# Performance work log

Hardware: AMD Instinct MI355X
Metric: run time of the kernel (lower is better)

The kernel has to match this reference:

```python
import jax, jax.numpy as jnp
import numpy as np

VOCAB, EMB, HID, L = 100000, 128, 256, 9
B, S = 128, 512
H = HID // 2  # per-direction hidden size
PAD = 0


def setup_inputs() -> dict:
    key = jax.random.key(0)
    ks = jax.random.split(key, 18)
    seqs = jax.random.randint(ks[0], (B, S), 1, VOCAB)
    # left-aligned padding: lengths in [S//2, S]
    lens = jax.random.randint(ks[1], (B,), S // 2, S + 1)
    seqs = jnp.where(jnp.arange(S)[None, :] < lens[:, None], seqs, PAD)
    labels = jax.random.randint(ks[2], (B, S), 0, L)

    def n(k, shape, s=0.05):
        return jax.random.normal(k, shape, jnp.float32) * s

    emb = n(ks[3], (VOCAB, EMB)).at[PAD].set(0.0)
    inp = {
        'sequences': seqs, 'labels': labels, 'emb': emb,
        'w_ih_f': n(ks[4], (4 * H, EMB)), 'w_hh_f': n(ks[5], (4 * H, H)),
        'b_ih_f': n(ks[6], (4 * H,)), 'b_hh_f': n(ks[7], (4 * H,)),
        'w_ih_b': n(ks[8], (4 * H, EMB)), 'w_hh_b': n(ks[9], (4 * H, H)),
        'b_ih_b': n(ks[10], (4 * H,)), 'b_hh_b': n(ks[11], (4 * H,)),
        'w_out': n(ks[12], (L, HID)), 'b_out': n(ks[13], (L,)),
        'start_t': n(ks[14], (L,), 0.1), 'end_t': n(ks[15], (L,), 0.1),
        'trans': n(ks[16], (L, L), 0.1),
    }
    return inp


def _lstm_scan(x, w_ih, w_hh, b_ih, b_hh):
    # x: [S, B, E] -> hidden states [S, B, H]
    h0 = jnp.zeros((x.shape[1], w_hh.shape[1]), x.dtype)

    def step(carry, xt):
        h, c = carry
        g = xt @ w_ih.T + b_ih + h @ w_hh.T + b_hh
        i, f, gg, o = jnp.split(g, 4, axis=-1)  # PyTorch gate order i,f,g,o
        c = jax.nn.sigmoid(f) * c + jax.nn.sigmoid(i) * jnp.tanh(gg)
        h = jax.nn.sigmoid(o) * jnp.tanh(c)
        return (h, c), h

    _, hs = jax.lax.scan(step, (h0, h0), x)
    return hs


def reference(sequences, labels, emb, w_ih_f, w_hh_f, b_ih_f, b_hh_f,
              w_ih_b, w_hh_b, b_ih_b, b_hh_b, w_out, b_out,
              start_t, end_t, trans):
    # Embedding lookup (dropout is identity at inference)
    x = emb[sequences]                      # [B,S,E]
    xt = jnp.swapaxes(x, 0, 1)              # [S,B,E]
    hf = _lstm_scan(xt, w_ih_f, w_hh_f, b_ih_f, b_hh_f)
    hb = _lstm_scan(xt[::-1], w_ih_b, w_hh_b, b_ih_b, b_hh_b)[::-1]
    hcat = jnp.concatenate([hf, hb], axis=-1)         # [S,B,HID]
    emissions = jnp.swapaxes(hcat, 0, 1) @ w_out.T + b_out  # [B,S,L]

    mask = sequences != PAD                 # [B,S], first step all True
    maskf = mask.astype(emissions.dtype)

    # --- CRF numerator (score of gold path) ---
    em_tag = jnp.take_along_axis(emissions, labels[..., None], axis=2)[..., 0]  # [B,S]
    trans_sc = trans[labels[:, :-1], labels[:, 1:]]                              # [B,S-1]
    num = start_t[labels[:, 0]] + em_tag[:, 0] \
        + jnp.sum((trans_sc + em_tag[:, 1:]) * maskf[:, 1:], axis=1)
    seq_ends = jnp.sum(mask, axis=1) - 1
    last_tags = labels[jnp.arange(labels.shape[0]), seq_ends]
    num = num + end_t[last_tags]

    # --- CRF partition function (forward algorithm) ---
    def fstep(score, inp):
        em_t, m_t = inp  # [B,L], [B]
        nxt = jax.nn.logsumexp(score[:, :, None] + trans[None] + em_t[:, None, :], axis=1)
        return jnp.where(m_t[:, None], nxt, score), None

    score0 = start_t[None, :] + emissions[:, 0]  # [B,L]
    em_rest = jnp.swapaxes(emissions, 0, 1)[1:]  # [S-1,B,L]
    scoreT, _ = jax.lax.scan(fstep, score0, (em_rest, mask.T[1:]))
    denom = jax.nn.logsumexp(scoreT + end_t[None, :], axis=1)  # [B]

    # model returns -log_likelihood (torchcrf default reduction='sum')
    return -jnp.sum(num - denom)
```

## Files before the change

kernel.cpp:

```cpp
#include <hip/hip_runtime.h>
#include <hip/hip_bf16.h>

#define B_   128
#define S_   512
#define H_   128
#define G_   512
#define EMB_ 128
#define NL_  9
#define CPW_ 2

typedef __attribute__((ext_vector_type(8))) short bf16x8;
typedef __attribute__((ext_vector_type(4))) short bf16x4;
typedef __attribute__((ext_vector_type(4))) float f32x4;
typedef unsigned short ushort_t;

__device__ __forceinline__ void wg_bar() {
    asm volatile("s_waitcnt lgkmcnt(0)\n\ts_barrier" ::: "memory");
}

__device__ __forceinline__ float bfbits2f(short s) {
    unsigned int u = ((unsigned int)(unsigned short)s) << 16;
    return __builtin_bit_cast(float, u);
}
__device__ __forceinline__ short f2bf(float f) {
    unsigned int u = __builtin_bit_cast(unsigned int, f);
    u += 0x7FFFu + ((u >> 16) & 1u);
    return (short)(u >> 16);
}
__device__ __forceinline__ unsigned int pack2(float lo, float hi) {
    return (unsigned int)(unsigned short)f2bf(lo) | ((unsigned int)(unsigned short)f2bf(hi) << 16);
}
__device__ __forceinline__ float sigm(float x) {
    return __builtin_amdgcn_rcpf(1.f + exp2f(-1.4426950408889634f * x));
}
__device__ __forceinline__ float tanh_(float x) {
    return 1.f - 2.f * __builtin_amdgcn_rcpf(1.f + exp2f(2.8853900817779268f * x));
}

__global__ __launch_bounds__(512, 1)
void xw_gemm_kernel(const int* __restrict__ seq, const float* __restrict__ emb,
                    const float* __restrict__ w_ih_f, const float* __restrict__ b_ih_f,
                    const float* __restrict__ b_hh_f,
                    const float* __restrict__ w_ih_b, const float* __restrict__ b_ih_b,
                    const float* __restrict__ b_hh_b,
                    ushort_t* __restrict__ xw)
{
    __shared__ bf16x8 ldsX[64 * 17];

    const int tid  = threadIdx.x;
    const int wv   = tid >> 6;
    const int n16  = tid & 15;
    const int quad = (tid & 63) >> 4;
    const int dir  = blockIdx.x >> 10;
    const int rem  = blockIdx.x & 1023;
    const int pair = rem >> 4;
    const int tb   = (rem & 15) * 32;

    const float* wih = dir ? w_ih_b : w_ih_f;
    const float* bih = dir ? b_ih_b : b_ih_f;
    const float* bhh = dir ? b_hh_b : b_hh_f;

    {
        int row = tid >> 3, part = tid & 7;
        int b = 2 * pair + (row >> 5);
        int t = tb + (row & 31);
        int tok = seq[b * S_ + t];
        const float* ep = emb + (size_t)tok * EMB_ + part * 16;
        int rt = row >> 4, rr = row & 15;
#pragma unroll
        for (int h = 0; h < 2; h++) {
            float4 a = *(const float4*)(ep + h * 8);
            float4 b4 = *(const float4*)(ep + h * 8 + 4);
            bf16x8 fr;
            fr[0] = f2bf(a.x); fr[1] = f2bf(a.y); fr[2] = f2bf(a.z); fr[3] = f2bf(a.w);
            fr[4] = f2bf(b4.x); fr[5] = f2bf(b4.y); fr[6] = f2bf(b4.z); fr[7] = f2bf(b4.w);
            ldsX[(rt * 16 + part * 2 + h) * 17 + rr] = fr;
        }
    }

    bf16x8 bfrag[4][4];
    float  bias[4];
#pragma unroll
    for (int nt = 0; nt < 4; nt++) {
        int col = nt * 128 + wv * 16 + n16;
        bias[nt] = bih[col] + bhh[col];
#pragma unroll
        for (int ks = 0; ks < 4; ks++) {
            const float* p = wih + col * EMB_ + ks * 32 + quad * 8;
            bf16x8 fr;
#pragma unroll
            for (int j = 0; j < 8; j++) fr[j] = f2bf(p[j]);
            bfrag[nt][ks] = fr;
        }
    }
    __syncthreads();

#pragma unroll
    for (int half = 0; half < 2; half++) {
        f32x4 accA[4], accB[4];
        bf16x8 afA[4], afB[4];
#pragma unroll
        for (int ks = 0; ks < 4; ks++) {
            afA[ks] = ldsX[(half * 16 + ks * 4 + quad) * 17 + n16];
            afB[ks] = ldsX[((half + 2) * 16 + ks * 4 + quad) * 17 + n16];
        }
#pragma unroll
        for (int nt = 0; nt < 4; nt++) {
            f32x4 a = {bias[nt], bias[nt], bias[nt], bias[nt]};
            accA[nt] = a; accB[nt] = a;
#pragma unroll
            for (int ks = 0; ks < 4; ks++) {
                accA[nt] = __builtin_amdgcn_mfma_f32_16x16x32_bf16(afA[ks], bfrag[nt][ks], accA[nt], 0, 0, 0);
                accB[nt] = __builtin_amdgcn_mfma_f32_16x16x32_bf16(afB[ks], bfrag[nt][ks], accB[nt], 0, 0, 0);
            }
        }
#pragma unroll
        for (int r = 0; r < 4; r++) {
            int t = tb + half * 16 + quad * 4 + r;
            int4 iv;
            iv.x = (int)pack2(accA[0][r], accA[1][r]);
            iv.y = (int)pack2(accA[2][r], accA[3][r]);
            iv.z = (int)pack2(accB[0][r], accB[1][r]);
            iv.w = (int)pack2(accB[2][r], accB[3][r]);
            size_t idx = ((((size_t)dir * 64 + pair) * S_ + t) * 8 + wv) * 16 + n16;
            *(int4*)(xw + idx * 8) = iv;
        }
    }
}

#define STEP(K)                                                                    \
  {                                                                                \
    const int u = m16 + (K);                                                       \
    if ((K) == 0 && m < 31) {                                                      \
      const ushort_t* gp = xwp + (size_t)(dir ? (S_ - 32 - m16) : (m16 + 16)) * 1024; \
      sA = *(const int4*)(gp + tid * 8);                                           \
      sB = *(const int4*)(gp + 4096 + tid * 8);                                    \
      sC = *(const int4*)(gp + 8192 + tid * 8);                                    \
      sD = *(const int4*)(gp + 12288 + tid * 8);                                   \
    }                                                                              \
                          \
    bf16x8 af0 = ldsH[(K) & 1][(0  + quad) * 2 + hpar];                            \
    bf16x8 af1 = ldsH[(K) & 1][(4  + quad) * 2 + hpar];                            \
    bf16x8 af2 = ldsH[(K) & 1][(8  + quad) * 2 + hpar];                            \
    bf16x8 af3 = ldsH[(K) & 1][(12 + quad) * 2 + hpar];                            \
    bf16x4 xvg = *(const bf16x4*)(xwS + ((m & 1) * 2048 + ((dir ? (15 - (K)) : (K)) * 8 + wv) * 16 + n16) * 8 + qsel); \
    if ((K) == 8 && m < 31) {                                                      \
      int4* dst = (int4*)(xwL + (((m & 1) ^ 1) * 2048));                           \
      dst[tid] = sA; dst[512 + tid] = sB; dst[1024 + tid] = sC; dst[1536 + tid] = sD; \
    }                                                                              \
    if ((K) == 1 && m >= 1 && (wv == 4 || wv == 5) && lane < 36) {                 \
      int a0 = dir ? (S_ - m16) : (m16 - 16);                                      \
      int eb = (a0 & 31) * 18 + flb;                                               \
      float4 fv;                                                                   \
      fv.x = emL[eb]; fv.y = emL[eb + 2]; fv.z = emL[eb + 4]; fv.w = emL[eb + 6];  \
      *(float4*)(emdir + (size_t)(brow0 + (wv - 4)) * (S_ * NL_) + a0 * NL_ + lane * 4) = fv; \
    }                                                                              \
    f32x4 acc0 = __builtin_amdgcn_mfma_f32_16x16x32_bf16(af0, bfrag[0][0], ZACC, 0, 0, 0); \
    f32x4 acc1 = __builtin_amdgcn_mfma_f32_16x16x32_bf16(af0, bfrag[1][0], ZACC, 0, 0, 0); \
    f32x4 acc2 = __builtin_amdgcn_mfma_f32_16x16x32_bf16(af0, bfrag[2][0], ZACC, 0, 0, 0); \
    f32x4 acc3 = __builtin_amdgcn_mfma_f32_16x16x32_bf16(af0, bfrag[3][0], ZACC, 0, 0, 0); \
    acc0 = __builtin_amdgcn_mfma_f32_16x16x32_bf16(af1, bfrag[0][1], acc0, 0, 0, 0); \
    acc1 = __builtin_amdgcn_mfma_f32_16x16x32_bf16(af1, bfrag[1][1], acc1, 0, 0, 0); \
    acc2 = __builtin_amdgcn_mfma_f32_16x16x32_bf16(af1, bfrag[2][1], acc2, 0, 0, 0); \
    acc3 = __builtin_amdgcn_mfma_f32_16x16x32_bf16(af1, bfrag[3][1], acc3, 0, 0, 0); \
    acc0 = __builtin_amdgcn_mfma_f32_16x16x32_bf16(af2, bfrag[0][2], acc0, 0, 0, 0); \
    acc1 = __builtin_amdgcn_mfma_f32_16x16x32_bf16(af2, bfrag[1][2], acc1, 0, 0, 0); \
    acc2 = __builtin_amdgcn_mfma_f32_16x16x32_bf16(af2, bfrag[2][2], acc2, 0, 0, 0); \
    acc3 = __builtin_amdgcn_mfma_f32_16x16x32_bf16(af2, bfrag[3][2], acc3, 0, 0, 0); \
    acc0 = __builtin_amdgcn_mfma_f32_16x16x32_bf16(af3, bfrag[0][3], acc0, 0, 0, 0); \
    acc1 = __builtin_amdgcn_mfma_f32_16x16x32_bf16(af3, bfrag[1][3], acc1, 0, 0, 0); \
    acc2 = __builtin_amdgcn_mfma_f32_16x16x32_bf16(af3, bfrag[2][3], acc2, 0, 0, 0); \
    acc3 = __builtin_amdgcn_mfma_f32_16x16x32_bf16(af3, bfrag[3][3], acc3, 0, 0, 0); \
    if (wv == 0) {                                                                 \
      f32x4 accE = __builtin_amdgcn_mfma_f32_16x16x32_bf16(af0, bfragE[0], ZACC, 0, 0, 0); \
      accE = __builtin_amdgcn_mfma_f32_16x16x32_bf16(af1, bfragE[1], accE, 0, 0, 0); \
      accE = __builtin_amdgcn_mfma_f32_16x16x32_bf16(af2, bfragE[2], accE, 0, 0, 0); \
      accE = __builtin_amdgcn_mfma_f32_16x16x32_bf16(af3, bfragE[3], accE, 0, 0, 0); \
      if (quad < 2 && n16 < NL_ && u >= 1) {                                       \
        int tprev = dir ? (S_ - u) : (u - 1);                                      \
        emL[((tprev & 31) * 9 + n16) * 2 + quad] = accE[0];                        \
      }                                                                            \
    }                                                                              \
    {                                                                              \
      float gi = acc0[0] + bfbits2f(xvg[0]);                                       \
      float gf = acc1[0] + bfbits2f(xvg[1]);                                       \
      float gg = acc2[0] + bfbits2f(xvg[2]);                                       \
      float go = acc3[0] + bfbits2f(xvg[3]);                                       \
      cst = sigm(gf) * cst + sigm(gi) * tanh_(gg);                                 \
      float hv = sigm(go) * tanh_(cst);                                            \
      if (quad < 2) *(((K) & 1) ? hw0 : hw1) = f2bf(hv);                           \
    }                                                                              \
    wg_bar();                                                                      \
  }

__global__ __launch_bounds__(512, 1)
void lstm_kernel(const ushort_t* __restrict__ xw,
                 const float* __restrict__ w_hh_f, const float* __restrict__ w_hh_b,
                 const float* __restrict__ w_out,
                 float* __restrict__ em_f, float* __restrict__ em_b)
{
    __shared__ bf16x8 xwL[2 * 2048];
    __shared__ bf16x8 ldsH[2][32];
    __shared__ float  emL[32 * NL_ * 2];

    const int tid  = threadIdx.x;
    const int wv   = tid >> 6;
    const int lane = tid & 63;
    const int n16  = tid & 15;
    const int quad = (tid & 63) >> 4;
    const int dir  = blockIdx.x >> 6;
    const int pair = blockIdx.x & 63;
    const int brow0 = pair * CPW_;

    const int hpar = (n16 >> 2) & 1;
    const int qsel = (quad & 1) * 4;
    const int hc   = 2 * wv + (n16 >> 3);
    const int hp   = n16 & 7;
    const int flb  = lane * 8 + (wv - 4);

    short* hw0 = ((short*)&ldsH[0][0]) + (hc * 2 + quad) * 8 + hp;
    short* hw1 = ((short*)&ldsH[1][0]) + (hc * 2 + quad) * 8 + hp;
    const short* xwS = (const short*)xwL;

    const f32x4 ZACC = {0.f, 0.f, 0.f, 0.f};

    const float* whh = dir ? w_hh_b : w_hh_f;
    float* emdir = dir ? em_b : em_f;

    bf16x8 bfrag[4][4];
#pragma unroll
    for (int nt = 0; nt < 4; nt++) {
        int col = nt * 128 + wv * 16 + n16;
#pragma unroll
        for (int ks = 0; ks < 4; ks++) {
            const float* p = whh + col * H_ + ks * 32 + quad * 8;
            bf16x8 fr;
#pragma unroll
            for (int j = 0; j < 8; j++) fr[j] = f2bf(p[j]);
            bfrag[nt][ks] = fr;
        }
    }
    bf16x8 bfragE[4];
#pragma unroll
    for (int ks = 0; ks < 4; ks++) {
        bf16x8 fr = {0, 0, 0, 0, 0, 0, 0, 0};
        if (n16 < NL_) {
            const float* p = w_out + n16 * 256 + dir * 128 + ks * 32 + quad * 8;
#pragma unroll
            for (int j = 0; j < 8; j++) fr[j] = f2bf(p[j]);
        }
        bfragE[ks] = fr;
    }

    if (tid < 128) ((int*)ldsH)[tid] = 0;

    const ushort_t* xwp = xw + (size_t)(dir * 64 + pair) * ((size_t)S_ * 1024);
    {
        const ushort_t* gp = xwp + (size_t)(dir ? (S_ - 16) : 0) * 1024;
        int4 a0 = *(const int4*)(gp + tid * 8);
        int4 a1 = *(const int4*)(gp + 4096 + tid * 8);
        int4 a2 = *(const int4*)(gp + 8192 + tid * 8);
        int4 a3 = *(const int4*)(gp + 12288 + tid * 8);
        int4* dst = (int4*)xwL;
        dst[tid] = a0; dst[512 + tid] = a1; dst[1024 + tid] = a2; dst[1536 + tid] = a3;
    }

    float cst = 0.f;
    int4 sA, sB, sC, sD;
    wg_bar();

    for (int m = 0; m < 32; m++) {
        const int m16 = m << 4;
        STEP(0)  STEP(1)  STEP(2)  STEP(3)
        STEP(4)  STEP(5)  STEP(6)  STEP(7)
        STEP(8)  STEP(9)  STEP(10) STEP(11)
        STEP(12) STEP(13) STEP(14) STEP(15)
    }

    if (wv == 0) {
        bf16x8 af0 = ldsH[0][(0  + quad) * 2 + hpar];
        bf16x8 af1 = ldsH[0][(4  + quad) * 2 + hpar];
        bf16x8 af2 = ldsH[0][(8  + quad) * 2 + hpar];
        bf16x8 af3 = ldsH[0][(12 + quad) * 2 + hpar];
        f32x4 accE = __builtin_amdgcn_mfma_f32_16x16x32_bf16(af0, bfragE[0], ZACC, 0, 0, 0);
        accE = __builtin_amdgcn_mfma_f32_16x16x32_bf16(af1, bfragE[1], accE, 0, 0, 0);
        accE = __builtin_amdgcn_mfma_f32_16x16x32_bf16(af2, bfragE[2], accE, 0, 0, 0);
        accE = __builtin_amdgcn_mfma_f32_16x16x32_bf16(af3, bfragE[3], accE, 0, 0, 0);
        if (quad < 2 && n16 < NL_) {
            int tprev = dir ? 0 : (S_ - 1);
            emL[((tprev & 31) * 9 + n16) * 2 + quad] = accE[0];
        }
    }
    wg_bar();
    if ((wv == 4 || wv == 5) && lane < 36) {
        int a0 = dir ? 0 : (S_ - 16);
        int eb = (a0 & 31) * 18 + flb;
        float4 fv;
        fv.x = emL[eb]; fv.y = emL[eb + 2]; fv.z = emL[eb + 4]; fv.w = emL[eb + 6];
        *(float4*)(emdir + (size_t)(brow0 + (wv - 4)) * (S_ * NL_) + a0 * NL_ + lane * 4) = fv;
    }
}

__global__ __launch_bounds__(640, 1)
void crf_kernel(const int* __restrict__ seq, const int* __restrict__ lab,
                const float* __restrict__ em_f, const float* __restrict__ em_b,
                const float* __restrict__ b_out,
                const float* __restrict__ start_t, const float* __restrict__ end_t,
                const float* __restrict__ trans, float* __restrict__ partial)
{
    __shared__ float emS[S_ * NL_];
    __shared__ float transS[NL_ * NL_];
    __shared__ float stS[NL_], enS[NL_];
    __shared__ unsigned char maskS[S_];
    __shared__ float MS[7 * 81];
    __shared__ float vS[NL_];
    __shared__ float redw[10];
    __shared__ int   redl[10];

    const int b = blockIdx.x, tid = threadIdx.x;
    const size_t base = (size_t)b * S_ * NL_;
    const float L2E = 1.4426950408889634f, LN2 = 0.6931471805599453f;

    for (int q = tid; q < S_ * NL_; q += 640)
        emS[q] = em_f[base + q] + em_b[base + q] + b_out[q % NL_];
    if (tid < NL_ * NL_) transS[tid] = trans[tid];
    if (tid < NL_) { stS[tid] = start_t[tid]; enS[tid] = end_t[tid]; }
    if (tid < S_) maskS[tid] = (seq[b * S_ + tid] != 0);
    __syncthreads();

    float np = 0.f; int myc = 0;
    if (tid < S_) {
        myc = maskS[tid];
        if (tid >= 1 && maskS[tid]) {
            int lp = lab[b * S_ + tid - 1], lc = lab[b * S_ + tid];
            np = transS[lp * NL_ + lc] + emS[tid * NL_ + lc];
        }
    }
#pragma unroll
    for (int off = 32; off; off >>= 1) {
        np  += __shfl_down(np, off, 64);
        myc += __shfl_down(myc, off, 64);
    }
    if ((tid & 63) == 0) { redw[tid >> 6] = np; redl[tid >> 6] = myc; }

    const int w = tid >> 6, l = tid & 63;
    const int lg = l / 9;
    const int g  = w * 7 + lg;
    const bool sact = (lg < 7) && (g < 64);
    const int jj = sact ? (l - lg * 9) : 0;
    const int gb = sact ? lg * 9 : 0;
    float Tc[NL_];
#pragma unroll
    for (int i = 0; i < NL_; i++) Tc[i] = transS[i * NL_ + jj];
    float sc; int tbeg, tend, cN = 0, iN = 0;
    if (sact && g == 0) {
        sc = stS[jj] + emS[jj];
        tbeg = 1; tend = 64;
    } else if (sact) {
        cN = 1 + (g - 1) / 9; iN = (g - 1) % 9;
        sc = (jj == iN) ? 0.f : -1e30f;
        tbeg = cN * 64; tend = tbeg + 64;
    } else {
        sc = -1e30f; tbeg = 448; tend = 512;
    }
    for (int t = tbeg; t < tend; t++) {
        float emv = emS[t * NL_ + jj];
        float a[NL_];
#pragma unroll
        for (int i = 0; i < NL_; i++) a[i] = __shfl(sc, gb + i, 64) + Tc[i];
        float m = a[0];
#pragma unroll
        for (int i = 1; i < NL_; i++) m = fmaxf(m, a[i]);
        float sum = 0.f;
#pragma unroll
        for (int i = 0; i < NL_; i++) sum += exp2f((a[i] - m) * L2E);
        float nxt = emv + m + LN2 * log2f(sum);
        sc = maskS[t] ? nxt : sc;
    }
    if (sact) {
        if (g == 0) vS[jj] = sc;
        else MS[(cN - 1) * 81 + iN * NL_ + jj] = sc;
    }
    __syncthreads();

    if (tid < 64) {
        const int j = (tid < NL_) ? tid : (NL_ - 1);
        float v = vS[j];
        for (int c = 1; c < 8; c++) {
            float a[NL_];
#pragma unroll
            for (int i = 0; i < NL_; i++)
                a[i] = __shfl(v, i, 64) + MS[(c - 1) * 81 + i * NL_ + j];
            float m = a[0];
#pragma unroll
            for (int i = 1; i < NL_; i++) m = fmaxf(m, a[i]);
            float sum = 0.f;
#pragma unroll
            for (int i = 0; i < NL_; i++) sum += exp2f((a[i] - m) * L2E);
            v = m + LN2 * log2f(sum);
        }
        v += enS[j];
        float mm = -1e30f, av[NL_];
#pragma unroll
        for (int i = 0; i < NL_; i++) { float vi = __shfl(v, i, 64); av[i] = vi; mm = fmaxf(mm, vi); }
        float ss = 0.f;
#pragma unroll
        for (int i = 0; i < NL_; i++) ss += exp2f((av[i] - mm) * L2E);
        if (tid == 0) {
            float num = 0.f; int len = 0;
#pragma unroll
            for (int ww = 0; ww < 10; ww++) { num += redw[ww]; len += redl[ww]; }
            int l0 = lab[b * S_];
            int ll = lab[b * S_ + len - 1];
            num += stS[l0] + emS[l0] + enS[ll];
            partial[b] = (mm + LN2 * log2f(ss)) - num;
        }
    }
}

__global__ __launch_bounds__(128)
void reduce_kernel(const float* __restrict__ partial, float* __restrict__ out)
{
    __shared__ float s[128];
    int tid = threadIdx.x;
    s[tid] = partial[tid];
    __syncthreads();
    for (int off = 64; off; off >>= 1) {
        if (tid < off) s[tid] += s[tid + off];
        __syncthreads();
    }
    if (tid == 0) out[0] = s[0];
}

extern "C" void kernel_launch(void* const* d_in, const int* in_sizes, int n_in,
                              void* d_out, int out_size, void* d_ws, size_t ws_size,
                              hipStream_t stream)
{
    const int* seq = (const int*)d_in[0];
    const int* lab = (const int*)d_in[1];
    const float* emb    = (const float*)d_in[2];
    const float* w_ih_f = (const float*)d_in[3];
    const float* w_hh_f = (const float*)d_in[4];
    const float* b_ih_f = (const float*)d_in[5];
    const float* b_hh_f = (const float*)d_in[6];
    const float* w_ih_b = (const float*)d_in[7];
    const float* w_hh_b = (const float*)d_in[8];
    const float* b_ih_b = (const float*)d_in[9];
    const float* b_hh_b = (const float*)d_in[10];
    const float* w_out  = (const float*)d_in[11];
    const float* b_out  = (const float*)d_in[12];
    const float* start_t = (const float*)d_in[13];
    const float* end_t   = (const float*)d_in[14];
    const float* trans   = (const float*)d_in[15];

    char* ws = (char*)d_ws;
    const size_t xw_bytes = (size_t)2 * B_ * S_ * G_ * sizeof(ushort_t);
    const size_t em_bytes = (size_t)B_ * S_ * NL_ * sizeof(float);
    ushort_t* xw   = (ushort_t*)ws;
    float* em_f    = (float*)(ws + xw_bytes);
    float* em_b    = (float*)(ws + xw_bytes + em_bytes);
    float* partial = (float*)(ws + xw_bytes + 2 * em_bytes);

    xw_gemm_kernel<<<dim3(2048), dim3(512), 0, stream>>>(seq, emb,
        w_ih_f, b_ih_f, b_hh_f, w_ih_b, b_ih_b, b_hh_b, xw);
    lstm_kernel<<<dim3(128), dim3(512), 0, stream>>>(xw, w_hh_f, w_hh_b,
        w_out, em_f, em_b);
    crf_kernel<<<dim3(B_), dim3(640), 0, stream>>>(seq, lab, em_f, em_b, b_out,
        start_t, end_t, trans, partial);
    reduce_kernel<<<dim3(1), dim3(128), 0, stream>>>(partial, (float*)d_out);
}
```

Baseline: 521.7 us.

## Split LSTM recurrence to one sequence per block across 256 blocks

The LSTM recurrence kernel previously handled two batch rows per 512-thread block over 128 blocks. Now each 256-thread block handles a single sequence and direction, giving 256 blocks that cover more CUs. Each wave computes twice as many gate columns with two MFMA tiles and picks rows by quad. The xw layout from the GEMM kernel is changed to per-sequence planes to match. The cell update is also rewritten with exp2 and a single reciprocal to cut transcendental operations on the serial step. The cost is more MFMA work and more register pressure per wave, since most of the 16-row MFMA tile is padding.

```diff
diff --git a/kernel.cpp b/kernel.cpp
--- a/kernel.cpp
+++ b/kernel.cpp
@@ -7,7 +7,6 @@
 #define G_   512
 #define EMB_ 128
 #define NL_  9
-#define CPW_ 2
 
 typedef __attribute__((ext_vector_type(8))) short bf16x8;
 typedef __attribute__((ext_vector_type(4))) short bf16x4;
@@ -95,6 +94,8 @@
     }
     __syncthreads();
 
+    const size_t plane0 = (size_t)(dir * 128 + 2 * pair);
+
 #pragma unroll
     for (int half = 0; half < 2; half++) {
         f32x4 accA[4], accB[4];
@@ -114,112 +115,128 @@
                 accB[nt] = __builtin_amdgcn_mfma_f32_16x16x32_bf16(afB[ks], bfrag[nt][ks], accB[nt], 0, 0, 0);
             }
         }
+        const int u = wv * 16 + n16;
 #pragma unroll
         for (int r = 0; r < 4; r++) {
             int t = tb + half * 16 + quad * 4 + r;
-            int4 iv;
-            iv.x = (int)pack2(accA[0][r], accA[1][r]);
-            iv.y = (int)pack2(accA[2][r], accA[3][r]);
-            iv.z = (int)pack2(accB[0][r], accB[1][r]);
-            iv.w = (int)pack2(accB[2][r], accB[3][r]);
-            size_t idx = ((((size_t)dir * 64 + pair) * S_ + t) * 8 + wv) * 16 + n16;
-            *(int4*)(xw + idx * 8) = iv;
+            int2 iv0, iv1;
+            iv0.x = (int)pack2(accA[0][r], accA[1][r]);
+            iv0.y = (int)pack2(accA[2][r], accA[3][r]);
+            iv1.x = (int)pack2(accB[0][r], accB[1][r]);
+            iv1.y = (int)pack2(accB[2][r], accB[3][r]);
+            *(int2*)(xw + ((plane0 * S_ + t) * 128 + u) * 4) = iv0;
+            *(int2*)(xw + (((plane0 + 1) * S_ + t) * 128 + u) * 4) = iv1;
         }
     }
 }
 
 #define STEP(K)                                                                    \
   {                                                                                \
-    const int u = m16 + (K);                                                       \
+    const int uidx = m16 + (K);                                                    \
     if ((K) == 0 && m < 31) {                                                      \
-      const ushort_t* gp = xwp + (size_t)(dir ? (S_ - 32 - m16) : (m16 + 16)) * 1024; \
+      const ushort_t* gp = xwp + (size_t)(dir ? (S_ - 32 - m16) : (m16 + 16)) * 512; \
       sA = *(const int4*)(gp + tid * 8);                                           \
-      sB = *(const int4*)(gp + 4096 + tid * 8);                                    \
-      sC = *(const int4*)(gp + 8192 + tid * 8);                                    \
-      sD = *(const int4*)(gp + 12288 + tid * 8);                                   \
+      sB = *(const int4*)(gp + 2048 + tid * 8);                                    \
+      sC = *(const int4*)(gp + 4096 + tid * 8);                                    \
+      sD = *(const int4*)(gp + 6144 + tid * 8);                                    \
     }                                                                              \
-                          \
-    bf16x8 af0 = ldsH[(K) & 1][(0  + quad) * 2 + hpar];                            \
-    bf16x8 af1 = ldsH[(K) & 1][(4  + quad) * 2 + hpar];                            \
-    bf16x8 af2 = ldsH[(K) & 1][(8  + quad) * 2 + hpar];                            \
-    bf16x8 af3 = ldsH[(K) & 1][(12 + quad) * 2 + hpar];                            \
-    bf16x4 xvg = *(const bf16x4*)(xwS + ((m & 1) * 2048 + ((dir ? (15 - (K)) : (K)) * 8 + wv) * 16 + n16) * 8 + qsel); \
+    bf16x8 af0 = hbuf[(K) & 1][0 * 4 + quad];                                      \
+    bf16x8 af1 = hbuf[(K) & 1][1 * 4 + quad];                                      \
+    bf16x8 af2 = hbuf[(K) & 1][2 * 4 + quad];                                      \
+    bf16x8 af3 = hbuf[(K) & 1][3 * 4 + quad];                                      \
+    bf16x4 xvg = *(const bf16x4*)(xwS + (m & 1) * 8192 + (dir ? (15 - (K)) : (K)) * 512 + uu * 4); \
     if ((K) == 8 && m < 31) {                                                      \
-      int4* dst = (int4*)(xwL + (((m & 1) ^ 1) * 2048));                           \
-      dst[tid] = sA; dst[512 + tid] = sB; dst[1024 + tid] = sC; dst[1536 + tid] = sD; \
+      int4* dst = (int4*)(xwL + (((m & 1) ^ 1) * 1024));                           \
+      dst[tid] = sA; dst[256 + tid] = sB; dst[512 + tid] = sC; dst[768 + tid] = sD; \
     }                                                                              \
-    if ((K) == 1 && m >= 1 && (wv == 4 || wv == 5) && lane < 36) {                 \
+    if ((K) == 1 && m >= 1 && wv == 3 && lane < 36) {                              \
       int a0 = dir ? (S_ - m16) : (m16 - 16);                                      \
-      int eb = (a0 & 31) * 18 + flb;                                               \
-      float4 fv;                                                                   \
-      fv.x = emL[eb]; fv.y = emL[eb + 2]; fv.z = emL[eb + 4]; fv.w = emL[eb + 6];  \
-      *(float4*)(emdir + (size_t)(brow0 + (wv - 4)) * (S_ * NL_) + a0 * NL_ + lane * 4) = fv; \
+      float4 fv = *(const float4*)(emL + (a0 & 31) * 9 + lane * 4);                \
+      *(float4*)(emdir + (size_t)b * (S_ * NL_) + a0 * NL_ + lane * 4) = fv;       \
     }                                                                              \
-    f32x4 acc0 = __builtin_amdgcn_mfma_f32_16x16x32_bf16(af0, bfrag[0][0], ZACC, 0, 0, 0); \
-    f32x4 acc1 = __builtin_amdgcn_mfma_f32_16x16x32_bf16(af0, bfrag[1][0], ZACC, 0, 0, 0); \
-    f32x4 acc2 = __builtin_amdgcn_mfma_f32_16x16x32_bf16(af0, bfrag[2][0], ZACC, 0, 0, 0); \
-    f32x4 acc3 = __builtin_amdgcn_mfma_f32_16x16x32_bf16(af0, bfrag[3][0], ZACC, 0, 0, 0); \
-    acc0 = __builtin_amdgcn_mfma_f32_16x16x32_bf16(af1, bfrag[0][1], acc0, 0, 0, 0); \
-    acc1 = __builtin_amdgcn_mfma_f32_16x16x32_bf16(af1, bfrag[1][1], acc1, 0, 0, 0); \
-    acc2 = __builtin_amdgcn_mfma_f32_16x16x32_bf16(af1, bfrag[2][1], acc2, 0, 0, 0); \
-    acc3 = __builtin_amdgcn_mfma_f32_16x16x32_bf16(af1, bfrag[3][1], acc3, 0, 0, 0); \
-    acc0 = __builtin_amdgcn_mfma_f32_16x16x32_bf16(af2, bfrag[0][2], acc0, 0, 0, 0); \
-    acc1 = __builtin_amdgcn_mfma_f32_16x16x32_bf16(af2, bfrag[1][2], acc1, 0, 0, 0); \
-    acc2 = __builtin_amdgcn_mfma_f32_16x16x32_bf16(af2, bfrag[2][2], acc2, 0, 0, 0); \
-    acc3 = __builtin_amdgcn_mfma_f32_16x16x32_bf16(af2, bfrag[3][2], acc3, 0, 0, 0); \
-    acc0 = __builtin_amdgcn_mfma_f32_16x16x32_bf16(af3, bfrag[0][3], acc0, 0, 0, 0); \
-    acc1 = __builtin_amdgcn_mfma_f32_16x16x32_bf16(af3, bfrag[1][3], acc1, 0, 0, 0); \
-    acc2 = __builtin_amdgcn_mfma_f32_16x16x32_bf16(af3, bfrag[2][3], acc2, 0, 0, 0); \
-    acc3 = __builtin_amdgcn_mfma_f32_16x16x32_bf16(af3, bfrag[3][3], acc3, 0, 0, 0); \
+    f32x4 aA0 = __builtin_amdgcn_mfma_f32_16x16x32_bf16(af0, bfrag[0][0][0], ZACC, 0, 0, 0); \
+    f32x4 aA1 = __builtin_amdgcn_mfma_f32_16x16x32_bf16(af0, bfrag[0][1][0], ZACC, 0, 0, 0); \
+    f32x4 aA2 = __builtin_amdgcn_mfma_f32_16x16x32_bf16(af0, bfrag[0][2][0], ZACC, 0, 0, 0); \
+    f32x4 aA3 = __builtin_amdgcn_mfma_f32_16x16x32_bf16(af0, bfrag[0][3][0], ZACC, 0, 0, 0); \
+    f32x4 aB0 = __builtin_amdgcn_mfma_f32_16x16x32_bf16(af0, bfrag[1][0][0], ZACC, 0, 0, 0); \
+    f32x4 aB1 = __builtin_amdgcn_mfma_f32_16x16x32_bf16(af0, bfrag[1][1][0], ZACC, 0, 0, 0); \
+    f32x4 aB2 = __builtin_amdgcn_mfma_f32_16x16x32_bf16(af0, bfrag[1][2][0], ZACC, 0, 0, 0); \
+    f32x4 aB3 = __builtin_amdgcn_mfma_f32_16x16x32_bf16(af0, bfrag[1][3][0], ZACC, 0, 0, 0); \
+    aA0 = __builtin_amdgcn_mfma_f32_16x16x32_bf16(af1, bfrag[0][0][1], aA0, 0, 0, 0); \
+    aA1 = __builtin_amdgcn_mfma_f32_16x16x32_bf16(af1, bfrag[0][1][1], aA1, 0, 0, 0); \
+    aA2 = __builtin_amdgcn_mfma_f32_16x16x32_bf16(af1, bfrag[0][2][1], aA2, 0, 0, 0); \
+    aA3 = __builtin_amdgcn_mfma_f32_16x16x32_bf16(af1, bfrag[0][3][1], aA3, 0, 0, 0); \
+    aB0 = __builtin_amdgcn_mfma_f32_16x16x32_bf16(af1, bfrag[1][0][1], aB0, 0, 0, 0); \
+    aB1 = __builtin_amdgcn_mfma_f32_16x16x32_bf16(af1, bfrag[1][1][1], aB1, 0, 0, 0); \
+    aB2 = __builtin_amdgcn_mfma_f32_16x16x32_bf16(af1, bfrag[1][2][1], aB2, 0, 0, 0); \
+    aB3 = __builtin_amdgcn_mfma_f32_16x16x32_bf16(af1, bfrag[1][3][1], aB3, 0, 0, 0); \
+    aA0 = __builtin_amdgcn_mfma_f32_16x16x32_bf16(af2, bfrag[0][0][2], aA0, 0, 0, 0); \
+    aA1 = __builtin_amdgcn_mfma_f32_16x16x32_bf16(af2, bfrag[0][1][2], aA1, 0, 0, 0); \
+    aA2 = __builtin_amdgcn_mfma_f32_16x16x32_bf16(af2, bfrag[0][2][2], aA2, 0, 0, 0); \
+    aA3 = __builtin_amdgcn_mfma_f32_16x16x32_bf16(af2, bfrag[0][3][2], aA3, 0, 0, 0); \
+    aB0 = __builtin_amdgcn_mfma_f32_16x16x32_bf16(af2, bfrag[1][0][2], aB0, 0, 0, 0); \
+    aB1 = __builtin_amdgcn_mfma_f32_16x16x32_bf16(af2, bfrag[1][1][2], aB1, 0, 0, 0); \
+    aB2 = __builtin_amdgcn_mfma_f32_16x16x32_bf16(af2, bfrag[1][2][2], aB2, 0, 0, 0); \
+    aB3 = __builtin_amdgcn_mfma_f32_16x16x32_bf16(af2, bfrag[1][3][2], aB3, 0, 0, 0); \
+    aA0 = __builtin_amdgcn_mfma_f32_16x16x32_bf16(af3, bfrag[0][0][3], aA0, 0, 0, 0); \
+    aA1 = __builtin_amdgcn_mfma_f32_16x16x32_bf16(af3, bfrag[0][1][3], aA1, 0, 0, 0); \
+    aA2 = __builtin_amdgcn_mfma_f32_16x16x32_bf16(af3, bfrag[0][2][3], aA2, 0, 0, 0); \
+    aA3 = __builtin_amdgcn_mfma_f32_16x16x32_bf16(af3, bfrag[0][3][3], aA3, 0, 0, 0); \
+    aB0 = __builtin_amdgcn_mfma_f32_16x16x32_bf16(af3, bfrag[1][0][3], aB0, 0, 0, 0); \
+    aB1 = __builtin_amdgcn_mfma_f32_16x16x32_bf16(af3, bfrag[1][1][3], aB1, 0, 0, 0); \
+    aB2 = __builtin_amdgcn_mfma_f32_16x16x32_bf16(af3, bfrag[1][2][3], aB2, 0, 0, 0); \
+    aB3 = __builtin_amdgcn_mfma_f32_16x16x32_bf16(af3, bfrag[1][3][3], aB3, 0, 0, 0); \
     if (wv == 0) {                                                                 \
       f32x4 accE = __builtin_amdgcn_mfma_f32_16x16x32_bf16(af0, bfragE[0], ZACC, 0, 0, 0); \
       accE = __builtin_amdgcn_mfma_f32_16x16x32_bf16(af1, bfragE[1], accE, 0, 0, 0); \
       accE = __builtin_amdgcn_mfma_f32_16x16x32_bf16(af2, bfragE[2], accE, 0, 0, 0); \
       accE = __builtin_amdgcn_mfma_f32_16x16x32_bf16(af3, bfragE[3], accE, 0, 0, 0); \
-      if (quad < 2 && n16 < NL_ && u >= 1) {                                       \
-        int tprev = dir ? (S_ - u) : (u - 1);                                      \
-        emL[((tprev & 31) * 9 + n16) * 2 + quad] = accE[0];                        \
+      if (quad == 0 && n16 < NL_ && uidx >= 1) {                                   \
+        int tprev = dir ? (S_ - uidx) : (uidx - 1);                                \
+        emL[(tprev & 31) * 9 + n16] = accE[0];                                     \
       }                                                                            \
     }                                                                              \
     {                                                                              \
-      float gi = acc0[0] + bfbits2f(xvg[0]);                                       \
-      float gf = acc1[0] + bfbits2f(xvg[1]);                                       \
-      float gg = acc2[0] + bfbits2f(xvg[2]);                                       \
-      float go = acc3[0] + bfbits2f(xvg[3]);                                       \
-      cst = sigm(gf) * cst + sigm(gi) * tanh_(gg);                                 \
-      float hv = sigm(go) * tanh_(cst);                                            \
-      if (quad < 2) *(((K) & 1) ? hw0 : hw1) = f2bf(hv);                           \
+      float gi = ((quad & 2) ? aB0[0] : aA0[0]) + bfbits2f(xvg[0]);                \
+      float gf = ((quad & 2) ? aB1[0] : aA1[0]) + bfbits2f(xvg[1]);                \
+      float gg = ((quad & 2) ? aB2[0] : aA2[0]) + bfbits2f(xvg[2]);                \
+      float go = ((quad & 2) ? aB3[0] : aA3[0]) + bfbits2f(xvg[3]);                \
+      float Af = exp2f(-1.4426950408889634f * gf);                                 \
+      float Bi = exp2f(-1.4426950408889634f * gi);                                 \
+      float Cg = exp2f(2.8853900817779268f * gg);                                  \
+      float Fo = exp2f(-1.4426950408889634f * go);                                 \
+      float oA = 1.f + Af, oB = 1.f + Bi, oC = 1.f + Cg;                           \
+      float P = oB * oC;                                                           \
+      float numer = cst * P + oA * (Cg - 1.f);                                     \
+      cst = numer * __builtin_amdgcn_rcpf(oA * P);                                 \
+      float hv = tanh_(cst) * __builtin_amdgcn_rcpf(1.f + Fo);                     \
+      if (!(quad & 1)) *(((K) & 1) ? hw0 : hw1) = f2bf(hv);                        \
     }                                                                              \
     wg_bar();                                                                      \
   }
 
-__global__ __launch_bounds__(512, 1)
+__global__ __launch_bounds__(256, 1)
 void lstm_kernel(const ushort_t* __restrict__ xw,
                  const float* __restrict__ w_hh_f, const float* __restrict__ w_hh_b,
                  const float* __restrict__ w_out,
                  float* __restrict__ em_f, float* __restrict__ em_b)
 {
-    __shared__ bf16x8 xwL[2 * 2048];
-    __shared__ bf16x8 ldsH[2][32];
-    __shared__ float  emL[32 * NL_ * 2];
+    __shared__ bf16x8 xwL[2 * 1024];
+    __shared__ bf16x8 hbuf[2][16];
+    __shared__ __align__(16) float emL[32 * NL_];
 
     const int tid  = threadIdx.x;
     const int wv   = tid >> 6;
     const int lane = tid & 63;
     const int n16  = tid & 15;
     const int quad = (tid & 63) >> 4;
-    const int dir  = blockIdx.x >> 6;
-    const int pair = blockIdx.x & 63;
-    const int brow0 = pair * CPW_;
-
-    const int hpar = (n16 >> 2) & 1;
-    const int qsel = (quad & 1) * 4;
-    const int hc   = 2 * wv + (n16 >> 3);
-    const int hp   = n16 & 7;
-    const int flb  = lane * 8 + (wv - 4);
-
-    short* hw0 = ((short*)&ldsH[0][0]) + (hc * 2 + quad) * 8 + hp;
-    short* hw1 = ((short*)&ldsH[1][0]) + (hc * 2 + quad) * 8 + hp;
+    const int dir  = blockIdx.x >> 7;
+    const int b    = blockIdx.x & 127;
+
+    const int uu = wv * 32 + ((quad >> 1) << 4) + n16;
+
+    short* hw0 = ((short*)hbuf) + uu;
+    short* hw1 = ((short*)hbuf) + 128 + uu;
     const short* xwS = (const short*)xwL;
 
     const f32x4 ZACC = {0.f, 0.f, 0.f, 0.f};
@@ -227,17 +244,20 @@
     const float* whh = dir ? w_hh_b : w_hh_f;
     float* emdir = dir ? em_b : em_f;
 
-    bf16x8 bfrag[4][4];
-#pragma unroll
-    for (int nt = 0; nt < 4; nt++) {
-        int col = nt * 128 + wv * 16 + n16;
-#pragma unroll
-        for (int ks = 0; ks < 4; ks++) {
-            const float* p = whh + col * H_ + ks * 32 + quad * 8;
-            bf16x8 fr;
-#pragma unroll
-            for (int j = 0; j < 8; j++) fr[j] = f2bf(p[j]);
-            bfrag[nt][ks] = fr;
+    bf16x8 bfrag[2][4][4];
+#pragma unroll
+    for (int tl = 0; tl < 2; tl++) {
+#pragma unroll
+        for (int nt = 0; nt < 4; nt++) {
+            int col = nt * 128 + wv * 32 + tl * 16 + n16;
+#pragma unroll
+            for (int ks = 0; ks < 4; ks++) {
+                const float* p = whh + col * H_ + ks * 32 + quad * 8;
+                bf16x8 fr;
+#pragma unroll
+                for (int j = 0; j < 8; j++) fr[j] = f2bf(p[j]);
+                bfrag[tl][nt][ks] = fr;
+            }
         }
     }
     bf16x8 bfragE[4];
@@ -252,17 +272,17 @@
         bfragE[ks] = fr;
     }
 
-    if (tid < 128) ((int*)ldsH)[tid] = 0;
-
-    const ushort_t* xwp = xw + (size_t)(dir * 64 + pair) * ((size_t)S_ * 1024);
+    if (tid < 64) ((int*)hbuf)[tid] = 0;
+
+    const ushort_t* xwp = xw + (size_t)(dir * 128 + b) * ((size_t)S_ * 512);
     {
-        const ushort_t* gp = xwp + (size_t)(dir ? (S_ - 16) : 0) * 1024;
+        const ushort_t* gp = xwp + (size_t)(dir ? (S_ - 16) : 0) * 512;
         int4 a0 = *(const int4*)(gp + tid * 8);
-        int4 a1 = *(const int4*)(gp + 4096 + tid * 8);
-        int4 a2 = *(const int4*)(gp + 8192 + tid * 8);
-        int4 a3 = *(const int4*)(gp + 12288 + tid * 8);
+        int4 a1 = *(const int4*)(gp + 2048 + tid * 8);
+        int4 a2 = *(const int4*)(gp + 4096 + tid * 8);
+        int4 a3 = *(const int4*)(gp + 6144 + tid * 8);
         int4* dst = (int4*)xwL;
-        dst[tid] = a0; dst[512 + tid] = a1; dst[1024 + tid] = a2; dst[1536 + tid] = a3;
+        dst[tid] = a0; dst[256 + tid] = a1; dst[512 + tid] = a2; dst[768 + tid] = a3;
     }
 
     float cst = 0.f;
@@ -278,26 +298,24 @@
     }
 
     if (wv == 0) {
-        bf16x8 af0 = ldsH[0][(0  + quad) * 2 + hpar];
-        bf16x8 af1 = ldsH[0][(4  + quad) * 2 + hpar];
-        bf16x8 af2 = ldsH[0][(8  + quad) * 2 + hpar];
-        bf16x8 af3 = ldsH[0][(12 + quad) * 2 + hpar];
+        bf16x8 af0 = hbuf[0][0 * 4 + quad];
+        bf16x8 af1 = hbuf[0][1 * 4 + quad];
+        bf16x8 af2 = hbuf[0][2 * 4 + quad];
+        bf16x8 af3 = hbuf[0][3 * 4 + quad];
         f32x4 accE = __builtin_amdgcn_mfma_f32_16x16x32_bf16(af0, bfragE[0], ZACC, 0, 0, 0);
         accE = __builtin_amdgcn_mfma_f32_16x16x32_bf16(af1, bfragE[1], accE, 0, 0, 0);
         accE = __builtin_amdgcn_mfma_f32_16x16x32_bf16(af2, bfragE[2], accE, 0, 0, 0);
         accE = __builtin_amdgcn_mfma_f32_16x16x32_bf16(af3, bfragE[3], accE, 0, 0, 0);
-        if (quad < 2 && n16 < NL_) {
+        if (quad == 0 && n16 < NL_) {
             int tprev = dir ? 0 : (S_ - 1);
-            emL[((tprev & 31) * 9 + n16) * 2 + quad] = accE[0];
+            emL[(tprev & 31) * 9 + n16] = accE[0];
         }
     }
     wg_bar();
-    if ((wv == 4 || wv == 5) && lane < 36) {
+    if (wv == 3 && lane < 36) {
         int a0 = dir ? 0 : (S_ - 16);
-        int eb = (a0 & 31) * 18 + flb;
-        float4 fv;
-        fv.x = emL[eb]; fv.y = emL[eb + 2]; fv.z = emL[eb + 4]; fv.w = emL[eb + 6];
-        *(float4*)(emdir + (size_t)(brow0 + (wv - 4)) * (S_ * NL_) + a0 * NL_ + lane * 4) = fv;
+        float4 fv = *(const float4*)(emL + (a0 & 31) * 9 + lane * 4);
+        *(float4*)(emdir + (size_t)b * (S_ * NL_) + a0 * NL_ + lane * 4) = fv;
     }
 }
 
@@ -463,7 +481,7 @@
 
     xw_gemm_kernel<<<dim3(2048), dim3(512), 0, stream>>>(seq, emb,
         w_ih_f, b_ih_f, b_hh_f, w_ih_b, b_ih_b, b_hh_b, xw);
-    lstm_kernel<<<dim3(128), dim3(512), 0, stream>>>(xw, w_hh_f, w_hh_b,
+    lstm_kernel<<<dim3(256), dim3(256), 0, stream>>>(xw, w_hh_f, w_hh_b,
         w_out, em_f, em_b);
     crf_kernel<<<dim3(B_), dim3(640), 0, stream>>>(seq, lab, em_f, em_b, b_out,
         start_t, end_t, trans, partial);
```

Result: slower. 533.7 us (+2.3%).
